# Performance work log

Measured on AMD Instinct MI355X. Metric: run time of the kernel, lower is better.

Reference implementation:

```python
import jax, jax.numpy as jnp
import numpy as np

B, NS, NT = 4, 512, 512
D_IN, C1, R, C2 = 128, 64, 32, 32
E = 32768
STEPS = 10


def setup_inputs() -> dict:
    key = jax.random.key(0)
    ks = jax.random.split(key, 12)
    inp = {}
    inp['x_s'] = jax.random.normal(ks[0], (B * NS, D_IN), jnp.float32)
    inp['edge_index_s'] = jax.random.randint(ks[1], (2, E), 0, B * NS, jnp.int32)
    inp['edge_attr_s'] = jax.random.uniform(ks[2], (E,), jnp.float32)
    inp['batch_s'] = (jnp.arange(B * NS, dtype=jnp.int32) // NS)
    inp['x_t'] = jax.random.normal(ks[3], (B * NT, D_IN), jnp.float32)
    inp['edge_index_t'] = jax.random.randint(ks[4], (2, E), 0, B * NT, jnp.int32)
    inp['edge_attr_t'] = jax.random.uniform(ks[5], (E,), jnp.float32)
    inp['batch_t'] = (jnp.arange(B * NT, dtype=jnp.int32) // NT)
    inp['W1'] = jax.random.normal(ks[6], (D_IN, C1), jnp.float32) / np.float32(np.sqrt(D_IN))
    inp['W2'] = jax.random.normal(ks[7], (R, C2), jnp.float32) / np.float32(np.sqrt(R))
    inp['mw1'] = jax.random.normal(ks[8], (C2, C2), jnp.float32) / np.float32(np.sqrt(C2))
    inp['mb1'] = jnp.zeros((C2,), jnp.float32)
    inp['mw2'] = jax.random.normal(ks[9], (C2, 1), jnp.float32) / np.float32(np.sqrt(C2))
    inp['mb2'] = jnp.zeros((1,), jnp.float32)
    inp['r'] = jax.random.normal(ks[10], (STEPS, B, NS, R), jnp.float32)
    return inp


def psi(x, src, dst, ea, W, n):
    # simple message-passing GNN: edge-weighted neighbor aggregation + linear + ReLU
    m = jax.ops.segment_sum(x[src] * ea[:, None], dst, num_segments=n)
    return jax.nn.relu((x + m) @ W)


def reference(x_s, edge_index_s, edge_attr_s, batch_s, x_t, edge_index_t, edge_attr_t,
              batch_t, W1, W2, mw1, mb1, mw2, mb2, r):
    # Uniform graph sizes -> to_dense_batch is a reshape and all masks are True,
    # so masked_softmax reduces to plain softmax; batch_s/batch_t kept for interface fidelity.
    ss, ds = edge_index_s[0], edge_index_s[1]
    st, dt = edge_index_t[0], edge_index_t[1]
    h_s = psi(x_s, ss, ds, edge_attr_s, W1, B * NS).reshape(B, NS, C1)
    h_t = psi(x_t, st, dt, edge_attr_t, W1, B * NT).reshape(B, NT, C1)
    S_hat0 = jnp.einsum('bsc,btc->bst', h_s, h_t)  # [B, NS, NT]
    S_0 = jax.nn.softmax(S_hat0, axis=-1)

    def step(S_hat, r_i):
        S = jax.nn.softmax(S_hat, axis=-1)
        r_t = jnp.einsum('bst,bsr->btr', S, r_i)  # S^T @ r_s
        o_s = psi(r_i.reshape(B * NS, R), ss, ds, edge_attr_s, W2, B * NS).reshape(B, NS, C2)
        o_t = psi(r_t.reshape(B * NT, R), st, dt, edge_attr_t, W2, B * NT).reshape(B, NT, C2)
        Dm = o_s[:, :, None, :] - o_t[:, None, :, :]  # [B, NS, NT, C2] outer difference
        upd = (jax.nn.relu(Dm @ mw1 + mb1) @ mw2 + mb2)[..., 0]
        return S_hat + upd, None

    S_hat, _ = jax.lax.scan(step, S_hat0, r)
    S_L = jax.nn.softmax(S_hat, axis=-1)
    return (S_0, S_L)
```

## Files before the change

### kernel.cpp

```cpp
#include <hip/hip_runtime.h>


constexpr int kB = 4;
constexpr int kNS = 512;
constexpr int kNT = 512;
constexpr int kDin = 128;
constexpr int kC1 = 64;
constexpr int kR = 32;
constexpr int kC2 = 32;
constexpr int kE = 32768;
constexpr int kSteps = 10;
constexpr int kN = kB * kNS;
constexpr int kEP = kE + 8 * kN;
constexpr int kChunkStride = kR * kN;

__global__ void k_hist(const int* __restrict__ ei_s, const int* __restrict__ ei_t,
                       int* __restrict__ deg) {
  int g = blockIdx.y;
  const int* dst = (g ? ei_t : ei_s) + kE;
  int e = blockIdx.x * 256 + threadIdx.x;
  atomicAdd(&deg[g * kN + dst[e]], 1);
}

__global__ void k_scan(const int* __restrict__ deg, int* __restrict__ off,
                       int* __restrict__ cur) {
  int g = blockIdx.x;
  const int* d = deg + g * kN;
  int* o = off + g * (kN + 1);
  int* c = cur + g * kN;
  __shared__ int sums[256];
  int tid = threadIdx.x;
  int loc[8];
  int s = 0;
#pragma unroll
  for (int i = 0; i < 8; ++i) {
    loc[i] = (d[tid * 8 + i] + 7) & ~7;
    s += loc[i];
  }
  sums[tid] = s;
  __syncthreads();
  for (int st = 1; st < 256; st <<= 1) {
    int v = (tid >= st) ? sums[tid - st] : 0;
    __syncthreads();
    sums[tid] += v;
    __syncthreads();
  }
  int base = (tid > 0) ? sums[tid - 1] : 0;
#pragma unroll
  for (int i = 0; i < 8; ++i) {
    int idx = tid * 8 + i;
    o[idx] = base;
    c[idx] = base;
    base += loc[i];
  }
  if (tid == 255) o[kN] = base;
}

__global__ void k_scatter(const int* __restrict__ ei_s, const int* __restrict__ ei_t,
                          const float* __restrict__ ea_s, const float* __restrict__ ea_t,
                          int* __restrict__ cur, int* __restrict__ srcs,
                          float* __restrict__ eaw) {
  int g = blockIdx.y;
  const int* ei = g ? ei_t : ei_s;
  const float* ea = g ? ea_t : ea_s;
  int e = blockIdx.x * 256 + threadIdx.x;
  int d = ei[kE + e];
  int srcv = ei[e];
  int pos = atomicAdd(&cur[g * kN + d], 1);
  srcs[g * kEP + pos] = srcv;
  eaw[g * kEP + pos] = ea[e];
}

__device__ __forceinline__ void psi2_node(
    int n, const float* __restrict__ vin, const int* __restrict__ sr,
    const float* __restrict__ ew, const int* __restrict__ o,
    const float* __restrict__ W2, const float* __restrict__ mw1,
    const float* __restrict__ mb1, float* __restrict__ Pout) {
  int lane = threadIdx.x & 63;
  int f = lane & 31, hh = lane >> 5;
  int beg = o[n], end = o[n + 1];
  float m = 0.f;
  for (int b0 = beg + hh * 4; b0 < end; b0 += 8) {
#pragma unroll
    for (int q = 0; q < 4; ++q)
      m += vin[(size_t)sr[b0 + q] * kR + f] * ew[b0 + q];
  }
  m += __shfl_down(m, 32, 64);
  float v = vin[(size_t)n * kR + f] + m;
  float acc = 0.f;
#pragma unroll
  for (int k = 0; k < kC2; ++k) acc += __shfl(v, k, 64) * W2[k * kC2 + f];
  float ov = fmaxf(acc, 0.f);
  float p = mb1 ? mb1[f] : 0.f;
#pragma unroll
  for (int k = 0; k < kC2; ++k) p += __shfl(ov, k, 64) * mw1[k * kC2 + f];
  if (lane < 32) Pout[(size_t)n * kC2 + f] = p;
}

__global__ __launch_bounds__(256) void k_pre(
    const float* __restrict__ x_s, const float* __restrict__ x_t,
    const float* __restrict__ r, const int* __restrict__ srcs,
    const float* __restrict__ eaw, const int* __restrict__ off,
    const float* __restrict__ W1, const float* __restrict__ W2,
    const float* __restrict__ mw1, const float* __restrict__ mb1,
    float* __restrict__ h, float* __restrict__ PsAll) {
  int bid = blockIdx.x, tid = threadIdx.x;
  if (bid < 2048) {
    int g = bid >> 10;
    int n = (bid & 1023) * 2 + (tid >> 7);
    int f = tid & 127;
    const float* x = g ? x_t : x_s;
    const int* sr = srcs + g * kEP;
    const float* ew = eaw + g * kEP;
    const int* o = off + g * (kN + 1);
    float* ho = h + (size_t)g * kN * kC1;
    __shared__ float y[2][kDin];
    int beg = o[n], end = o[n + 1];
    float m = 0.f;
    for (int idx = beg; idx < end; idx += 2) {
      float m2 = x[(size_t)sr[idx + 1] * kDin + f] * ew[idx + 1];
      m += x[(size_t)sr[idx] * kDin + f] * ew[idx];
      m += m2;
    }
    y[tid >> 7][f] = x[(size_t)n * kDin + f] + m;
    __syncthreads();
    if (f < kC1) {
      const float* yy = y[tid >> 7];
      float acc = 0.f;
#pragma unroll 16
      for (int k = 0; k < kDin; ++k) acc += yy[k] * W1[k * kC1 + f];
      ho[(size_t)n * kC1 + f] = fmaxf(acc, 0.f);
    }
  } else {
    int nn = (bid - 2048) * 4 + (tid >> 6);
    int step = nn >> 11, node = nn & (kN - 1);
    psi2_node(node, r + (size_t)step * kN * kR, srcs, eaw, off, W2, mw1, mb1,
              PsAll + (size_t)step * kN * kR);
  }
}

__global__ __launch_bounds__(256) void k_shat0(const float* __restrict__ h,
                                               float* __restrict__ Shat,
                                               float* __restrict__ pstatm,
                                               float* __restrict__ pstatl) {
  int b = blockIdx.z, s0 = blockIdx.y * 64, t0 = blockIdx.x * 64;
  const float* hs = h + (size_t)(b * kNS + s0) * kC1;
  const float* ht = h + (size_t)kN * kC1 + (size_t)(b * kNT + t0) * kC1;
  __shared__ float As[64 * 68];
  __shared__ float Bs[64 * 68];
  int tid = threadIdx.x;
#pragma unroll
  for (int k2 = 0; k2 < 4; ++k2) {
    int idx = tid + k2 * 256;
    int row = idx >> 4, c4 = idx & 15;
    float4 va = *(const float4*)(hs + (size_t)row * kC1 + c4 * 4);
    *(float4*)&As[row * 68 + c4 * 4] = va;
    float4 vb = *(const float4*)(ht + (size_t)row * kC1 + c4 * 4);
    *(float4*)&Bs[row * 68 + c4 * 4] = vb;
  }
  __syncthreads();
  int ts = tid >> 4, tt = tid & 15;
  float acc[4][4] = {};
#pragma unroll
  for (int cc = 0; cc < 16; ++cc) {
    float4 a[4], bt[4];
#pragma unroll
    for (int i = 0; i < 4; ++i) a[i] = *(const float4*)&As[(ts * 4 + i) * 68 + cc * 4];
#pragma unroll
    for (int k = 0; k < 4; ++k) bt[k] = *(const float4*)&Bs[(tt + 16 * k) * 68 + cc * 4];
#pragma unroll
    for (int i = 0; i < 4; ++i)
#pragma unroll
      for (int k = 0; k < 4; ++k)
        acc[i][k] += a[i].x * bt[k].x + a[i].y * bt[k].y + a[i].z * bt[k].z + a[i].w * bt[k].w;
  }
#pragma unroll
  for (int i = 0; i < 4; ++i) {
    int s = s0 + ts * 4 + i;
    float* row = Shat + (size_t)(b * kNS + s) * kNT;
#pragma unroll
    for (int k = 0; k < 4; ++k) row[t0 + tt + 16 * k] = acc[i][k];
  }
#pragma unroll
  for (int i = 0; i < 4; ++i) {
    float mm = fmaxf(fmaxf(acc[i][0], acc[i][1]), fmaxf(acc[i][2], acc[i][3]));
#pragma unroll
    for (int o2 = 8; o2; o2 >>= 1) mm = fmaxf(mm, __shfl_xor(mm, o2, 64));
    float se = 0.f;
#pragma unroll
    for (int k = 0; k < 4; ++k) se += __expf(acc[i][k] - mm);
#pragma unroll
    for (int o2 = 8; o2; o2 >>= 1) se += __shfl_xor(se, o2, 64);
    if (tt == 0) {
      int grow = b * kNS + s0 + ts * 4 + i;
      pstatm[blockIdx.x * kN + grow] = mm;
      pstatl[blockIdx.x * kN + grow] = se;
    }
  }
}

__global__ __launch_bounds__(256) void k_rt(const float* __restrict__ Shat,
                                            const float* __restrict__ pstatm,
                                            const float* __restrict__ pstatl,
                                            const float* __restrict__ ri,
                                            float* __restrict__ part, int nc,
                                            float* __restrict__ Sout) {
  int b = blockIdx.z, cs = blockIdx.y, s0 = cs * 64, t0 = blockIdx.x * 64;
  __shared__ float Wt[64 * 64];
  __shared__ float rch[64 * 32];
  __shared__ float lm[64], ll[64];
  int tid = threadIdx.x;
  if (tid < 64) {
    int row = b * kNS + s0 + tid;
    float m = -3.4e38f;
    for (int c = 0; c < nc; ++c) m = fmaxf(m, pstatm[c * kN + row]);
    float l = 0.f;
    for (int c = 0; c < nc; ++c) l += __expf(pstatm[c * kN + row] - m) * pstatl[c * kN + row];
    lm[tid] = m;
    ll[tid] = 1.f / l;
  }
  __syncthreads();
#pragma unroll
  for (int k2 = 0; k2 < 4; ++k2) {
    int idx = tid + k2 * 256;
    int row = idx >> 4, c4 = idx & 15;
    int grow = b * kNS + s0 + row;
    float4 v = *(const float4*)(Shat + (size_t)grow * kNT + t0 + c4 * 4);
    float m = lm[row], l = ll[row];
    float4 wv;
    wv.x = __expf(v.x - m) * l;
    wv.y = __expf(v.y - m) * l;
    wv.z = __expf(v.z - m) * l;
    wv.w = __expf(v.w - m) * l;
    *(float4*)&Wt[row * 64 + c4 * 4] = wv;
    if (Sout) *(float4*)(Sout + (size_t)grow * kNT + t0 + c4 * 4) = wv;
  }
#pragma unroll
  for (int k2 = 0; k2 < 2; ++k2) {
    int idx = tid + k2 * 256;
    int row = idx >> 3, c4 = idx & 7;
    float4 v = *(const float4*)(ri + (size_t)(b * kNS + s0 + row) * kR + c4 * 4);
    *(float4*)&rch[row * 32 + c4 * 4] = v;
  }
  __syncthreads();
  int t_l = tid & 63, jg = tid >> 6;
  float acc[8] = {};
  for (int s = 0; s < 64; ++s) {
    float wv = Wt[s * 64 + t_l];
    float4 ra = *(const float4*)&rch[s * 32 + jg * 8];
    float4 rb = *(const float4*)&rch[s * 32 + jg * 8 + 4];
    acc[0] += wv * ra.x; acc[1] += wv * ra.y; acc[2] += wv * ra.z; acc[3] += wv * ra.w;
    acc[4] += wv * rb.x; acc[5] += wv * rb.y; acc[6] += wv * rb.z; acc[7] += wv * rb.w;
  }
  int gcol = b * kNT + t0 + t_l;
  float* dst = part + (size_t)cs * kChunkStride + (size_t)jg * 8 * kN + gcol;
#pragma unroll
  for (int q = 0; q < 8; ++q) dst[(size_t)q * kN] = acc[q];
}

__global__ __launch_bounds__(256) void k_red(const float* __restrict__ part,
                                             float* __restrict__ rt) {
  int idx = blockIdx.x * 256 + threadIdx.x;
  int j = idx >> 11, col = idx & (kN - 1);
  float s = 0.f;
#pragma unroll
  for (int cs = 0; cs < 8; ++cs) s += part[(size_t)cs * kChunkStride + idx];
  rt[(size_t)col * kR + j] = s;
}

__global__ __launch_bounds__(256) void k_psi2t(
    const float* __restrict__ rt, const int* __restrict__ srcs,
    const float* __restrict__ eaw, const int* __restrict__ off,
    const float* __restrict__ W2, const float* __restrict__ mw1,
    float* __restrict__ Pt) {
  int n = blockIdx.x * 4 + (threadIdx.x >> 6);
  psi2_node(n, rt, srcs + kEP, eaw + kEP, off + (kN + 1), W2, mw1, nullptr, Pt);
}

__global__ __launch_bounds__(256) void k_upd(
    float* __restrict__ Shat, const float* __restrict__ Ps,
    const float* __restrict__ Pt, const float* __restrict__ mw2,
    const float* __restrict__ mb2, float* __restrict__ pstatm,
    float* __restrict__ pstatl) {
  __shared__ float pts[256 * 33];
  __shared__ float red[8 * 4];
  __shared__ float lmx[8];
  int tid = threadIdx.x;
  int g0 = blockIdx.x * 8;
  int cc = blockIdx.y;
  int bb = g0 >> 9;
  int c0 = cc * 256;
  const float4* PtB = (const float4*)(Pt + ((size_t)bb * kNT + c0) * kC2);
#pragma unroll
  for (int k = 0; k < 8; ++k) {
    int idx = tid + k * 256;
    int col = idx >> 3, q = idx & 7;
    float4 v = PtB[idx];
    float* d = &pts[col * 33 + q * 4];
    d[0] = v.x; d[1] = v.y; d[2] = v.z; d[3] = v.w;
  }
  float old[8];
#pragma unroll
  for (int s = 0; s < 8; ++s) old[s] = Shat[(size_t)(g0 + s) * kNT + c0 + tid];
  __syncthreads();
  float pt[32];
#pragma unroll
  for (int j = 0; j < 32; ++j) pt[j] = pts[tid * 33 + j];
  float bias = mb2[0];
  float nv[8];
#pragma unroll
  for (int s = 0; s < 8; ++s) {
    const float* psr = Ps + (size_t)(g0 + s) * kC2;
    float u = 0.f;
#pragma unroll
    for (int j = 0; j < 32; ++j) u += fmaxf(psr[j] - pt[j], 0.f) * mw2[j];
    float v = old[s] + u + bias;
    Shat[(size_t)(g0 + s) * kNT + c0 + tid] = v;
    nv[s] = v;
  }
  int wv = tid >> 6, ln = tid & 63;
#pragma unroll
  for (int s = 0; s < 8; ++s) {
    float m = nv[s];
#pragma unroll
    for (int o2 = 32; o2; o2 >>= 1) m = fmaxf(m, __shfl_down(m, o2, 64));
    if (ln == 0) red[s * 4 + wv] = m;
  }
  __syncthreads();
  if (tid < 8) {
    lmx[tid] = fmaxf(fmaxf(red[tid * 4], red[tid * 4 + 1]),
                     fmaxf(red[tid * 4 + 2], red[tid * 4 + 3]));
  }
  __syncthreads();
#pragma unroll
  for (int s = 0; s < 8; ++s) {
    float e = __expf(nv[s] - lmx[s]);
#pragma unroll
    for (int o2 = 32; o2; o2 >>= 1) e += __shfl_down(e, o2, 64);
    if (ln == 0) red[s * 4 + wv] = e;
  }
  __syncthreads();
  if (tid < 8) {
    float l = red[tid * 4] + red[tid * 4 + 1] + red[tid * 4 + 2] + red[tid * 4 + 3];
    pstatm[cc * kN + g0 + tid] = lmx[tid];
    pstatl[cc * kN + g0 + tid] = l;
  }
}

__global__ __launch_bounds__(256) void k_out(const float* __restrict__ Shat,
                                             const float* __restrict__ pstatm,
                                             const float* __restrict__ pstatl,
                                             float* __restrict__ out) {
  int row = blockIdx.x, tid = threadIdx.x;
  float m0 = pstatm[row], m1 = pstatm[kN + row];
  float l0 = pstatl[row], l1 = pstatl[kN + row];
  float m = fmaxf(m0, m1);
  float linv = 1.f / (__expf(m0 - m) * l0 + __expf(m1 - m) * l1);
  const float* p = Shat + (size_t)row * kNT;
  float* d = out + (size_t)row * kNT;
  d[tid] = __expf(p[tid] - m) * linv;
  d[tid + 256] = __expf(p[tid + 256] - m) * linv;
}

extern "C" void kernel_launch(void* const* d_in, const int* in_sizes, int n_in,
                              void* d_out, int out_size, void* d_ws, size_t ws_size,
                              hipStream_t stream) {
  (void)in_sizes; (void)n_in; (void)out_size; (void)ws_size;
  const float* x_s = (const float*)d_in[0];
  const int* ei_s = (const int*)d_in[1];
  const float* ea_s = (const float*)d_in[2];
  const float* x_t = (const float*)d_in[4];
  const int* ei_t = (const int*)d_in[5];
  const float* ea_t = (const float*)d_in[6];
  const float* W1 = (const float*)d_in[8];
  const float* W2 = (const float*)d_in[9];
  const float* mw1 = (const float*)d_in[10];
  const float* mb1 = (const float*)d_in[11];
  const float* mw2 = (const float*)d_in[12];
  const float* mb2 = (const float*)d_in[13];
  const float* r = (const float*)d_in[14];
  float* out = (float*)d_out;

  char* w = (char*)d_ws;
  auto alloc = [&](size_t bytes) -> void* {
    void* p = (void*)w;
    w += (bytes + 255) & ~(size_t)255;
    return p;
  };
  int* deg = (int*)alloc((size_t)2 * kN * 4);
  int* cur = (int*)alloc((size_t)2 * kN * 4);
  int* srcs = (int*)alloc((size_t)2 * kEP * 4);
  float* eaw = (float*)alloc((size_t)2 * kEP * 4);
  size_t zbytes = (size_t)((char*)(eaw + 2 * kEP) - (char*)deg);
  int* off = (int*)alloc((size_t)2 * (kN + 1) * 4);
  float* h = (float*)alloc((size_t)2 * kN * kC1 * 4);
  float* Shat = (float*)alloc((size_t)kB * kNS * kNT * 4);
  float* pstatm = (float*)alloc((size_t)8 * kN * 4);
  float* pstatl = (float*)alloc((size_t)8 * kN * 4);
  float* rt = (float*)alloc((size_t)kN * kR * 4);
  float* PsAll = (float*)alloc((size_t)kSteps * kN * kR * 4);
  float* Pt = (float*)alloc((size_t)kN * kC2 * 4);
  float* part = (float*)alloc((size_t)8 * kChunkStride * 4);

  hipMemsetAsync(deg, 0, zbytes, stream);
  k_hist<<<dim3(kE / 256, 2), 256, 0, stream>>>(ei_s, ei_t, deg);
  k_scan<<<2, 256, 0, stream>>>(deg, off, cur);
  k_scatter<<<dim3(kE / 256, 2), 256, 0, stream>>>(ei_s, ei_t, ea_s, ea_t, cur, srcs, eaw);
  k_pre<<<7168, 256, 0, stream>>>(x_s, x_t, r, srcs, eaw, off, W1, W2, mw1, mb1,
                                  h, PsAll);
  k_shat0<<<dim3(8, 8, kB), 256, 0, stream>>>(h, Shat, pstatm, pstatl);
  k_rt<<<dim3(8, 8, kB), 256, 0, stream>>>(Shat, pstatm, pstatl, r, part, 8, out);
  k_red<<<kChunkStride / 256, 256, 0, stream>>>(part, rt);
  for (int i = 0; i < kSteps; ++i) {
    k_psi2t<<<kN / 4, 256, 0, stream>>>(rt, srcs, eaw, off, W2, mw1, Pt);
    k_upd<<<dim3(kN / 8, 2), 256, 0, stream>>>(Shat, PsAll + (size_t)i * kN * kR, Pt,
                                               mw2, mb2, pstatm, pstatl);
    if (i + 1 < kSteps) {
      k_rt<<<dim3(8, 8, kB), 256, 0, stream>>>(Shat, pstatm, pstatl,
                                               r + (size_t)(i + 1) * kN * kR, part,
                                               2, nullptr);
      k_red<<<kChunkStride / 256, 256, 0, stream>>>(part, rt);
    }
  }
  k_out<<<kN, 256, 0, stream>>>(Shat, pstatm, pstatl, out + (size_t)kB * kNS * kNT);
}
```

Measured before the change: 445.9 us.

## Fuse partial-sum reduction of r_t into psi2 target kernel, drop k_red

Removes the separate k_red launch by having k_psi2t sum the 8 chunk partials directly while gathering neighbours, and changes the partial layout to node-major so k_rt writes float4 and the gathers are contiguous. The psi2 target kernel is rewritten to split edges across two half-wavefronts and combine them with a shuffle. The first-layer aggregation loop is unrolled by 4 with the self term hoisted. This saves 10 launches and an intermediate round trip, at the cost of reading 8 partials per neighbour edge (redundant reads, roughly 8x the gather traffic).

```diff
diff --git a/kernel.cpp b/kernel.cpp
--- a/kernel.cpp
+++ b/kernel.cpp
@@ -116,13 +116,16 @@
     float* ho = h + (size_t)g * kN * kC1;
     __shared__ float y[2][kDin];
     int beg = o[n], end = o[n + 1];
+    float xself = x[(size_t)n * kDin + f];
     float m = 0.f;
-    for (int idx = beg; idx < end; idx += 2) {
-      float m2 = x[(size_t)sr[idx + 1] * kDin + f] * ew[idx + 1];
-      m += x[(size_t)sr[idx] * kDin + f] * ew[idx];
-      m += m2;
+    for (int idx = beg; idx < end; idx += 4) {
+      float a0 = x[(size_t)sr[idx + 0] * kDin + f] * ew[idx + 0];
+      float a1 = x[(size_t)sr[idx + 1] * kDin + f] * ew[idx + 1];
+      float a2 = x[(size_t)sr[idx + 2] * kDin + f] * ew[idx + 2];
+      float a3 = x[(size_t)sr[idx + 3] * kDin + f] * ew[idx + 3];
+      m += (a0 + a1) + (a2 + a3);
     }
-    y[tid >> 7][f] = x[(size_t)n * kDin + f] + m;
+    y[tid >> 7][f] = xself + m;
     __syncthreads();
     if (f < kC1) {
       const float* yy = y[tid >> 7];
@@ -253,28 +256,49 @@
     acc[4] += wv * rb.x; acc[5] += wv * rb.y; acc[6] += wv * rb.z; acc[7] += wv * rb.w;
   }
   int gcol = b * kNT + t0 + t_l;
-  float* dst = part + (size_t)cs * kChunkStride + (size_t)jg * 8 * kN + gcol;
-#pragma unroll
-  for (int q = 0; q < 8; ++q) dst[(size_t)q * kN] = acc[q];
-}
-
-__global__ __launch_bounds__(256) void k_red(const float* __restrict__ part,
-                                             float* __restrict__ rt) {
-  int idx = blockIdx.x * 256 + threadIdx.x;
-  int j = idx >> 11, col = idx & (kN - 1);
-  float s = 0.f;
-#pragma unroll
-  for (int cs = 0; cs < 8; ++cs) s += part[(size_t)cs * kChunkStride + idx];
-  rt[(size_t)col * kR + j] = s;
+  float* dst = part + (size_t)cs * kChunkStride + (size_t)gcol * kR + jg * 8;
+  *(float4*)dst = make_float4(acc[0], acc[1], acc[2], acc[3]);
+  *(float4*)(dst + 4) = make_float4(acc[4], acc[5], acc[6], acc[7]);
 }
 
 __global__ __launch_bounds__(256) void k_psi2t(
-    const float* __restrict__ rt, const int* __restrict__ srcs,
+    const float* __restrict__ part, const int* __restrict__ srcs,
     const float* __restrict__ eaw, const int* __restrict__ off,
     const float* __restrict__ W2, const float* __restrict__ mw1,
     float* __restrict__ Pt) {
   int n = blockIdx.x * 4 + (threadIdx.x >> 6);
-  psi2_node(n, rt, srcs + kEP, eaw + kEP, off + (kN + 1), W2, mw1, nullptr, Pt);
+  int lane = threadIdx.x & 63;
+  int f = lane & 31, hh = lane >> 5;
+  const int* sr = srcs + kEP;
+  const float* ew = eaw + kEP;
+  const int* o = off + (kN + 1);
+  int beg = o[n], end = o[n + 1];
+  float m = 0.f;
+  for (int b0 = beg + hh * 4; b0 < end; b0 += 8) {
+#pragma unroll
+    for (int q = 0; q < 4; ++q) {
+      int rr = sr[b0 + q];
+      float v = 0.f;
+#pragma unroll
+      for (int cs = 0; cs < 8; ++cs)
+        v += part[(size_t)cs * kChunkStride + (size_t)rr * kR + f];
+      m += v * ew[b0 + q];
+    }
+  }
+  m += __shfl_down(m, 32, 64);
+  float vown = 0.f;
+#pragma unroll
+  for (int cs = 0; cs < 8; ++cs)
+    vown += part[(size_t)cs * kChunkStride + (size_t)n * kR + f];
+  float v = vown + m;
+  float acc = 0.f;
+#pragma unroll
+  for (int k = 0; k < kC2; ++k) acc += __shfl(v, k, 64) * W2[k * kC2 + f];
+  float ov = fmaxf(acc, 0.f);
+  float p = 0.f;
+#pragma unroll
+  for (int k = 0; k < kC2; ++k) p += __shfl(ov, k, 64) * mw1[k * kC2 + f];
+  if (lane < 32) Pt[(size_t)n * kC2 + f] = p;
 }
 
 __global__ __launch_bounds__(256) void k_upd(
@@ -397,7 +421,6 @@
   float* Shat = (float*)alloc((size_t)kB * kNS * kNT * 4);
   float* pstatm = (float*)alloc((size_t)8 * kN * 4);
   float* pstatl = (float*)alloc((size_t)8 * kN * 4);
-  float* rt = (float*)alloc((size_t)kN * kR * 4);
   float* PsAll = (float*)alloc((size_t)kSteps * kN * kR * 4);
   float* Pt = (float*)alloc((size_t)kN * kC2 * 4);
   float* part = (float*)alloc((size_t)8 * kChunkStride * 4);
@@ -410,16 +433,14 @@
                                   h, PsAll);
   k_shat0<<<dim3(8, 8, kB), 256, 0, stream>>>(h, Shat, pstatm, pstatl);
   k_rt<<<dim3(8, 8, kB), 256, 0, stream>>>(Shat, pstatm, pstatl, r, part, 8, out);
-  k_red<<<kChunkStride / 256, 256, 0, stream>>>(part, rt);
   for (int i = 0; i < kSteps; ++i) {
-    k_psi2t<<<kN / 4, 256, 0, stream>>>(rt, srcs, eaw, off, W2, mw1, Pt);
+    k_psi2t<<<kN / 4, 256, 0, stream>>>(part, srcs, eaw, off, W2, mw1, Pt);
     k_upd<<<dim3(kN / 8, 2), 256, 0, stream>>>(Shat, PsAll + (size_t)i * kN * kR, Pt,
                                                mw2, mb2, pstatm, pstatl);
     if (i + 1 < kSteps) {
       k_rt<<<dim3(8, 8, kB), 256, 0, stream>>>(Shat, pstatm, pstatl,
                                                r + (size_t)(i + 1) * kN * kR, part,
                                                2, nullptr);
-      k_red<<<kChunkStride / 256, 256, 0, stream>>>(part, rt);
     }
   }
   k_out<<<kN, 256, 0, stream>>>(Shat, pstatm, pstatl, out + (size_t)kB * kNS * kNT);
```

Measured after the change: 457.0 us. 2.5% more time.
